# Performance work log

Measured on AMD Instinct MI355X. Metric: run time of the kernel, lower is better.

The kernel has to match this reference:

```python
import jax, jax.numpy as jnp
import numpy as np

N_NODES = 100000
N_EDGES = 1600000
IN_FEATS = 256
N_HEADS = 4
OUT_FEATS = 32
NEG_SLOPE = 0.2


def setup_inputs() -> dict:
    key = jax.random.key(0)
    k0, k1, k2, k3, k4, k5 = jax.random.split(key, 6)
    feat = jax.random.normal(k0, (N_NODES, IN_FEATS), dtype=jnp.float32)
    src = jax.random.randint(k1, (N_EDGES,), 0, N_NODES, dtype=jnp.int32)
    dst = jax.random.randint(k2, (N_EDGES,), 0, N_NODES, dtype=jnp.int32)
    # fc.weight: [num_heads*out_feats, in_feats] (torch Linear layout)
    W = jax.random.normal(k3, (N_HEADS * OUT_FEATS, IN_FEATS), dtype=jnp.float32) * 0.05
    attn_l = jax.random.normal(k4, (1, N_HEADS, OUT_FEATS), dtype=jnp.float32) * 0.1
    attn_r = jax.random.normal(k5, (1, N_HEADS, OUT_FEATS), dtype=jnp.float32) * 0.1
    return {"feat": feat, "src": src, "dst": dst, "W": W, "attn_l": attn_l, "attn_r": attn_r}


def reference(feat, src, dst, W, attn_l, attn_r):
    N = feat.shape[0]
    H, D = attn_l.shape[1], attn_l.shape[2]
    # fc projection -> [N, H, D]
    feat_src = (feat @ W.T).reshape(N, H, D)
    el = jnp.sum(feat_src * attn_l, axis=-1)  # [N, H]
    er = jnp.sum(feat_src * attn_r, axis=-1)  # [N, H]
    # per-edge scores: u_add_v then LeakyReLU  -> [E, H]
    e = jax.nn.leaky_relu(el[src] + er[dst], negative_slope=NEG_SLOPE)
    # edge_softmax: segmented softmax over edges grouped by destination node
    emax = jax.ops.segment_max(e, dst, num_segments=N)  # [N, H]
    emax = jnp.where(jnp.isfinite(emax), emax, jnp.zeros_like(emax))
    ee = jnp.exp(e - emax[dst])  # [E, H]
    denom = jax.ops.segment_sum(ee, dst, num_segments=N)  # [N, H]
    a = ee / denom[dst]  # [E, H]
    # u_mul_e + sum aggregation -> [N, H, D]
    m = feat_src[src] * a[:, :, None]  # [E, H, D]
    rst = jax.ops.segment_sum(m, dst, num_segments=N)
    return rst
```

## Files before the change

kernel.cpp:

```cpp
#include <hip/hip_runtime.h>
#include <hip/hip_bf16.h>
#include <math.h>

#define NN 100000
#define NE 1600000
#define INF_ 256
#define NH 4
#define DH 32
#define NHD 128
#define NEG_SLOPE 0.2f

#define NB 391
#define EPB 8192
#define NBLK_H 196
#define GEMM_BLKS 782

typedef __attribute__((ext_vector_type(8))) short bf16x8;
typedef __attribute__((ext_vector_type(4))) float f32x4;

__device__ __forceinline__ unsigned short f2bf(float f) {
    __hip_bfloat16 b = __float2bfloat16(f);
    return *reinterpret_cast<unsigned short*>(&b);
}

__global__ __launch_bounds__(256) void k_wcvt(const float* __restrict__ W,
                                              unsigned short* __restrict__ Wimg) {
    int i = blockIdx.x * 256 + threadIdx.x;
    if (i >= 4096) return;
    int kt = i >> 9;
    int r = (i >> 2) & 127;
    int g = i & 3;
    int slot = g ^ (r & 7);
    const float* s = &W[(size_t)r * INF_ + kt * 32 + g * 8];
    unsigned short tmp[8];
#pragma unroll
    for (int j = 0; j < 8; j++) tmp[j] = f2bf(s[j]);
    *(bf16x8*)&Wimg[(size_t)kt * 8192 + r * 64 + slot * 8] = *(const bf16x8*)tmp;
}

__global__ __launch_bounds__(256) void k_gemm(const float* __restrict__ feat,
                                              const unsigned short* __restrict__ Wimg,
                                              const int* __restrict__ dst,
                                              const float* __restrict__ al,
                                              const float* __restrict__ ar,
                                              unsigned short* __restrict__ fsb,
                                              float* __restrict__ el,
                                              float* __restrict__ er,
                                              int* __restrict__ bcnt) {
    __shared__ short sA[128 * 64];
    __shared__ short sB[128 * 64];
    __shared__ int lh[NB];
    const int t = threadIdx.x;

    if (blockIdx.x >= GEMM_BLKS) {
        int hb = blockIdx.x - GEMM_BLKS;
        for (int i = t; i < NB; i += 256) lh[i] = 0;
        __syncthreads();
        int base = hb * EPB;
#pragma unroll
        for (int j = 0; j < 32; j++) {
            int e = base + j * 256 + t;
            if (e < NE) atomicAdd(&lh[dst[e] >> 8], 1);
        }
        __syncthreads();
        for (int i = t; i < NB; i += 256)
            if (lh[i]) atomicAdd(&bcnt[i], lh[i]);
        return;
    }

    const int brow = blockIdx.x * 128;
    const int wid = t >> 6, lane = t & 63;
    const int wr = wid >> 1, wc = wid & 1;
    const int lg = lane >> 4;
    const int lr = lane & 15;

    f32x4 acc[4][4];
#pragma unroll
    for (int m = 0; m < 4; m++)
#pragma unroll
        for (int n = 0; n < 4; n++) acc[m][n] = (f32x4){0.f, 0.f, 0.f, 0.f};

    const int srow = t >> 1;
    const int cb = (t & 1) * 16;
    const int g0 = cb >> 3;
    const int p0 = (g0 ^ (srow & 7));
    const int p1 = ((g0 + 1) ^ (srow & 7));
    const int grow = brow + srow;
    const bool arow_ok = (grow < NN);
    const char* bimg = (const char*)Wimg;

    float fv[16];
    uint4 wv0, wv1, wv2, wv3;
    if (arow_ok) {
        const float4* pa = (const float4*)&feat[(size_t)grow * INF_ + cb];
        *(float4*)&fv[0] = pa[0];
        *(float4*)&fv[4] = pa[1];
        *(float4*)&fv[8] = pa[2];
        *(float4*)&fv[12] = pa[3];
    } else {
#pragma unroll
        for (int j = 0; j < 16; j++) fv[j] = 0.f;
    }
    wv0 = *(const uint4*)(bimg + t * 16);
    wv1 = *(const uint4*)(bimg + 4096 + t * 16);
    wv2 = *(const uint4*)(bimg + 8192 + t * 16);
    wv3 = *(const uint4*)(bimg + 12288 + t * 16);

    for (int kt = 0; kt < 8; kt++) {
        {
            short sv[16];
#pragma unroll
            for (int j = 0; j < 16; j++) sv[j] = (short)f2bf(fv[j]);
            *(bf16x8*)&sA[srow * 64 + p0 * 8] = *(const bf16x8*)&sv[0];
            *(bf16x8*)&sA[srow * 64 + p1 * 8] = *(const bf16x8*)&sv[8];
            char* bd = (char*)sB;
            *(uint4*)(bd + t * 16) = wv0;
            *(uint4*)(bd + 4096 + t * 16) = wv1;
            *(uint4*)(bd + 8192 + t * 16) = wv2;
            *(uint4*)(bd + 12288 + t * 16) = wv3;
        }
        __syncthreads();
        if (kt < 7) {
            int k0 = (kt + 1) * 32;
            if (arow_ok) {
                const float4* pa = (const float4*)&feat[(size_t)grow * INF_ + k0 + cb];
                *(float4*)&fv[0] = pa[0];
                *(float4*)&fv[4] = pa[1];
                *(float4*)&fv[8] = pa[2];
                *(float4*)&fv[12] = pa[3];
            }
            const char* bsrc = bimg + (size_t)(kt + 1) * 16384;
            wv0 = *(const uint4*)(bsrc + t * 16);
            wv1 = *(const uint4*)(bsrc + 4096 + t * 16);
            wv2 = *(const uint4*)(bsrc + 8192 + t * 16);
            wv3 = *(const uint4*)(bsrc + 12288 + t * 16);
        }
        bf16x8 aF[4], bF[4];
#pragma unroll
        for (int m = 0; m < 4; m++) {
            int r = wr * 64 + m * 16 + lr;
            aF[m] = *(const bf16x8*)&sA[r * 64 + ((lg ^ (r & 7)) * 8)];
        }
#pragma unroll
        for (int n = 0; n < 4; n++) {
            int r = wc * 64 + n * 16 + lr;
            bF[n] = *(const bf16x8*)&sB[r * 64 + ((lg ^ (r & 7)) * 8)];
        }
#pragma unroll
        for (int m = 0; m < 4; m++)
#pragma unroll
            for (int n = 0; n < 4; n++)
                acc[m][n] = __builtin_amdgcn_mfma_f32_16x16x32_bf16(aF[m], bF[n], acc[m][n], 0, 0, 0);
        __syncthreads();
    }
#pragma unroll
    for (int m = 0; m < 4; m++) {
#pragma unroll
        for (int n = 0; n < 4; n++) {
#pragma unroll
            for (int r = 0; r < 4; r++) {
                int gr = brow + wr * 64 + m * 16 + lg * 4 + r;
                if (gr < NN)
                    fsb[(size_t)gr * NHD + wc * 64 + n * 16 + lr] = f2bf(acc[m][n][r]);
            }
        }
    }
    const int hA = wc * 2, hB = wc * 2 + 1;
    const float alA0 = al[hA * 32 + lr], alA1 = al[hA * 32 + 16 + lr];
    const float alB0 = al[hB * 32 + lr], alB1 = al[hB * 32 + 16 + lr];
    const float arA0 = ar[hA * 32 + lr], arA1 = ar[hA * 32 + 16 + lr];
    const float arB0 = ar[hB * 32 + lr], arB1 = ar[hB * 32 + 16 + lr];
#pragma unroll
    for (int m = 0; m < 4; m++) {
#pragma unroll
        for (int r = 0; r < 4; r++) {
            float eA = acc[m][0][r] * alA0 + acc[m][1][r] * alA1;
            float eB = acc[m][2][r] * alB0 + acc[m][3][r] * alB1;
            float fA = acc[m][0][r] * arA0 + acc[m][1][r] * arA1;
            float fB = acc[m][2][r] * arB0 + acc[m][3][r] * arB1;
#pragma unroll
            for (int off = 1; off < 16; off <<= 1) {
                eA += __shfl_xor(eA, off);
                eB += __shfl_xor(eB, off);
                fA += __shfl_xor(fA, off);
                fB += __shfl_xor(fB, off);
            }
            if (lr == 0) {
                int gr = brow + wr * 64 + m * 16 + lg * 4 + r;
                if (gr < NN) {
                    el[gr * 4 + hA] = eA;
                    el[gr * 4 + hB] = eB;
                    er[gr * 4 + hA] = fA;
                    er[gr * 4 + hB] = fB;
                }
            }
        }
    }
}

__global__ __launch_bounds__(512) void k_bscan(const int* __restrict__ bcnt,
                                               int* __restrict__ ebase,
                                               int* __restrict__ gcur) {
    __shared__ int s[512];
    int t = threadIdx.x;
    int v = (t < NB) ? bcnt[t] : 0;
    s[t] = v;
    __syncthreads();
#pragma unroll
    for (int off = 1; off < 512; off <<= 1) {
        int y = (t >= off) ? s[t - off] : 0;
        __syncthreads();
        s[t] += y;
        __syncthreads();
    }
    if (t < NB) {
        int e = s[t] - v;
        ebase[t] = e;
        gcur[t] = e;
    }
}

__global__ __launch_bounds__(256) void k_bin(const int* __restrict__ src,
                                             const int* __restrict__ dst,
                                             int* __restrict__ gcur,
                                             unsigned* __restrict__ packed) {
    __shared__ int ldst[EPB];
    __shared__ int lc[NB];
    __shared__ int wb[NB];
    int t = threadIdx.x;
    for (int i = t; i < NB; i += 256) lc[i] = 0;
    __syncthreads();
    int base = blockIdx.x * EPB;
#pragma unroll
    for (int j = 0; j < 32; j++) {
        int e = base + j * 256 + t;
        int d = (e < NE) ? dst[e] : -1;
        ldst[j * 256 + t] = d;
        if (d >= 0) atomicAdd(&lc[d >> 8], 1);
    }
    __syncthreads();
    for (int i = t; i < NB; i += 256) {
        int c = lc[i];
        wb[i] = c ? atomicAdd(&gcur[i], c) : 0;
        lc[i] = 0;
    }
    __syncthreads();
#pragma unroll
    for (int j = 0; j < 32; j++) {
        int e = base + j * 256 + t;
        if (e < NE) {
            int d = ldst[j * 256 + t];
            int b = d >> 8;
            int s = src[e];
            int pos = wb[b] + atomicAdd(&lc[b], 1);
            packed[pos] = ((unsigned)s << 8) | (unsigned)(d & 255);
        }
    }
}

__global__ __launch_bounds__(256) void k_sort(const int* __restrict__ ebase,
                                              const int* __restrict__ bcnt,
                                              const unsigned* __restrict__ packed,
                                              int* __restrict__ row_off,
                                              int* __restrict__ esrc) {
    __shared__ int lh[256];
    __shared__ int cur[256];
    __shared__ int wsum[4];
    int b = blockIdx.x, t = threadIdx.x;
    int beg = ebase[b];
    int end = beg + bcnt[b];
    lh[t] = 0;
    __syncthreads();
    for (int k = beg + t; k < end; k += 256) {
        atomicAdd(&lh[packed[k] & 255u], 1);
    }
    __syncthreads();
    int v = lh[t];
    int lane = t & 63, w = t >> 6;
    int x = v;
#pragma unroll
    for (int off = 1; off < 64; off <<= 1) {
        int y = __shfl_up(x, off);
        if (lane >= off) x += y;
    }
    if (lane == 63) wsum[w] = x;
    __syncthreads();
    int add = 0;
    for (int j = 0; j < w; j++) add += wsum[j];
    int excl = beg + add + x - v;
    int node = (b << 8) + t;
    if (node < NN) row_off[node] = excl;
    cur[t] = excl;
    __syncthreads();
    for (int k = beg + t; k < end; k += 256) {
        unsigned p = packed[k];
        int pos = atomicAdd(&cur[p & 255u], 1);
        esrc[pos] = (int)(p >> 8);
    }
    if (b == NB - 1 && t == 0) row_off[NN] = NE;
}

__global__ __launch_bounds__(256) void k_agg(const int* __restrict__ row_off,
                                             const int* __restrict__ esrc,
                                             const float* __restrict__ el,
                                             const float* __restrict__ er,
                                             const uint4* __restrict__ fsb128,
                                             float* __restrict__ out) {
    int gid = blockIdx.x * blockDim.x + threadIdx.x;
    int node = gid >> 6;
    int lane = gid & 63;
    if (node >= NN) return;
    int q = lane >> 4;
    int sl = lane & 15;
    int h = sl >> 2;
    int beg = row_off[node];
    int end = row_off[node + 1];
    float rr = er[node * 4 + h];
    float den = 0.f;
    float a0 = 0.f, a1 = 0.f, a2 = 0.f, a3 = 0.f;
    float a4 = 0.f, a5 = 0.f, a6 = 0.f, a7 = 0.f;

#define STEP(eV, vV)                                           \
    {                                                          \
        float sc = (eV) + rr;                                  \
        sc = sc > 0.f ? sc : NEG_SLOPE * sc;                   \
        float ee = __expf(sc);                                 \
        den += ee;                                             \
        a0 += ee * __uint_as_float((vV).x << 16);              \
        a1 += ee * __uint_as_float((vV).x & 0xFFFF0000u);      \
        a2 += ee * __uint_as_float((vV).y << 16);              \
        a3 += ee * __uint_as_float((vV).y & 0xFFFF0000u);      \
        a4 += ee * __uint_as_float((vV).z << 16);              \
        a5 += ee * __uint_as_float((vV).z & 0xFFFF0000u);      \
        a6 += ee * __uint_as_float((vV).w << 16);              \
        a7 += ee * __uint_as_float((vV).w & 0xFFFF0000u);      \
    }

    int k = beg + q;
    for (; k + 4 < end; k += 8) {
        int s0 = esrc[k];
        int s1 = esrc[k + 4];
        uint4 v0 = fsb128[(size_t)s0 * 16 + sl];
        uint4 v1 = fsb128[(size_t)s1 * 16 + sl];
        float e0 = el[s0 * 4 + h];
        float e1 = el[s1 * 4 + h];
        STEP(e0, v0)
        STEP(e1, v1)
    }
    for (; k < end; k += 4) {
        int s = esrc[k];
        uint4 v = fsb128[(size_t)s * 16 + sl];
        float eV = el[s * 4 + h];
        STEP(eV, v)
    }
#undef STEP

#pragma unroll
    for (int off = 16; off <= 32; off <<= 1) {
        a0 += __shfl_xor(a0, off);
        a1 += __shfl_xor(a1, off);
        a2 += __shfl_xor(a2, off);
        a3 += __shfl_xor(a3, off);
        a4 += __shfl_xor(a4, off);
        a5 += __shfl_xor(a5, off);
        a6 += __shfl_xor(a6, off);
        a7 += __shfl_xor(a7, off);
        den += __shfl_xor(den, off);
    }

    if (q == 0) {
        float inv = den > 0.f ? 1.0f / den : 0.f;
        float4 o0, o1;
        o0.x = a0 * inv; o0.y = a1 * inv; o0.z = a2 * inv; o0.w = a3 * inv;
        o1.x = a4 * inv; o1.y = a5 * inv; o1.z = a6 * inv; o1.w = a7 * inv;
        float* p = &out[(size_t)node * NHD + sl * 8];
        *(float4*)p = o0;
        *(float4*)(p + 4) = o1;
    }
}

extern "C" void kernel_launch(void* const* d_in, const int* in_sizes, int n_in,
                              void* d_out, int out_size, void* d_ws, size_t ws_size,
                              hipStream_t stream) {
    const float* feat = (const float*)d_in[0];
    const int* src = (const int*)d_in[1];
    const int* dst = (const int*)d_in[2];
    const float* W = (const float*)d_in[3];
    const float* al = (const float*)d_in[4];
    const float* ar = (const float*)d_in[5];
    float* out = (float*)d_out;

    char* ws = (char*)d_ws;
    unsigned short* fsb = (unsigned short*)ws;   ws += (size_t)NN * NHD * 2;
    unsigned* packed = (unsigned*)ws;            ws += (size_t)NE * 4;
    int* esrc = (int*)ws;                        ws += (size_t)NE * 4;
    float* el = (float*)ws;                      ws += (size_t)NN * NH * 4;
    float* er = (float*)ws;                      ws += (size_t)NN * NH * 4;
    int* row_off = (int*)ws;                     ws += (size_t)(NN + 1) * 4;
    int* bcnt = (int*)ws;                        ws += (size_t)NB * 4;
    int* ebase = (int*)ws;                       ws += (size_t)NB * 4;
    int* gcur = (int*)ws;                        ws += (size_t)NB * 4;
    unsigned short* Wimg = (unsigned short*)ws;  ws += (size_t)8 * 8192 * 2;

    hipMemsetAsync(bcnt, 0, (size_t)NB * sizeof(int), stream);

    k_wcvt<<<16, 256, 0, stream>>>(W, Wimg);
    k_gemm<<<GEMM_BLKS + NBLK_H, 256, 0, stream>>>(feat, Wimg, dst, al, ar,
                                                   fsb, el, er, bcnt);
    k_bscan<<<1, 512, 0, stream>>>(bcnt, ebase, gcur);
    k_bin<<<NBLK_H, 256, 0, stream>>>(src, dst, gcur, packed);
    k_sort<<<NB, 256, 0, stream>>>(ebase, bcnt, packed, row_off, esrc);
    k_agg<<<(NN * 64 + 255) / 256, 256, 0, stream>>>(row_off, esrc, el, er,
                                                     (const uint4*)fsb, out);
}
```

Measured before the change: 166.9 us.

## Fuse bucket scan into binning and local sort into aggregation

Removes the separate scan, sort and aggregation kernels by computing bucket prefix sums inside each binning block and doing per-bucket counting sort in shared memory directly before aggregation. Buckets shrink to 128 nodes so the sorted source list fits in LDS, eliminating the global esrc/row_off round trip and several launches. It also replaces the memset with a block in the weight-convert kernel. Risks include truncation if a bucket exceeds the fixed LDS capacity and reduced parallelism since each wave now serially handles 32 nodes.

Result: faster. 160.4 us (-3.9%).

```diff
diff --git a/kernel.cpp b/kernel.cpp
--- a/kernel.cpp
+++ b/kernel.cpp
@@ -10,10 +10,11 @@
 #define NHD 128
 #define NEG_SLOPE 0.2f
 
-#define NB 391
-#define EPB 8192
-#define NBLK_H 196
+#define NB2 782
+#define EPB 4096
+#define NBLK_H 391
 #define GEMM_BLKS 782
+#define MAXBE 3072
 
 typedef __attribute__((ext_vector_type(8))) short bf16x8;
 typedef __attribute__((ext_vector_type(4))) float f32x4;
@@ -23,10 +24,20 @@
     return *reinterpret_cast<unsigned short*>(&b);
 }
 
-__global__ __launch_bounds__(256) void k_wcvt(const float* __restrict__ W,
-                                              unsigned short* __restrict__ Wimg) {
-    int i = blockIdx.x * 256 + threadIdx.x;
-    if (i >= 4096) return;
+__global__ __launch_bounds__(256) void k_prep0(const float* __restrict__ W,
+                                               unsigned short* __restrict__ Wimg,
+                                               int* __restrict__ bcnt,
+                                               int* __restrict__ gcur) {
+    int t = threadIdx.x;
+    int b = blockIdx.x;
+    if (b == 16) {
+        for (int i = t; i < NB2; i += 256) {
+            bcnt[i] = 0;
+            gcur[i] = 0;
+        }
+        return;
+    }
+    int i = b * 256 + t;
     int kt = i >> 9;
     int r = (i >> 2) & 127;
     int g = i & 3;
@@ -49,21 +60,21 @@
                                               int* __restrict__ bcnt) {
     __shared__ short sA[128 * 64];
     __shared__ short sB[128 * 64];
-    __shared__ int lh[NB];
+    __shared__ int lh[NB2];
     const int t = threadIdx.x;
 
     if (blockIdx.x >= GEMM_BLKS) {
         int hb = blockIdx.x - GEMM_BLKS;
-        for (int i = t; i < NB; i += 256) lh[i] = 0;
+        for (int i = t; i < NB2; i += 256) lh[i] = 0;
         __syncthreads();
         int base = hb * EPB;
 #pragma unroll
-        for (int j = 0; j < 32; j++) {
+        for (int j = 0; j < 16; j++) {
             int e = base + j * 256 + t;
-            if (e < NE) atomicAdd(&lh[dst[e] >> 8], 1);
+            if (e < NE) atomicAdd(&lh[dst[e] >> 7], 1);
         }
         __syncthreads();
-        for (int i = t; i < NB; i += 256)
+        for (int i = t; i < NB2; i += 256)
             if (lh[i]) atomicAdd(&bcnt[i], lh[i]);
         return;
     }
@@ -198,133 +209,132 @@
     }
 }
 
-__global__ __launch_bounds__(512) void k_bscan(const int* __restrict__ bcnt,
-                                               int* __restrict__ ebase,
-                                               int* __restrict__ gcur) {
-    __shared__ int s[512];
-    int t = threadIdx.x;
-    int v = (t < NB) ? bcnt[t] : 0;
-    s[t] = v;
-    __syncthreads();
-#pragma unroll
-    for (int off = 1; off < 512; off <<= 1) {
-        int y = (t >= off) ? s[t - off] : 0;
-        __syncthreads();
-        s[t] += y;
-        __syncthreads();
-    }
-    if (t < NB) {
-        int e = s[t] - v;
-        ebase[t] = e;
-        gcur[t] = e;
-    }
-}
-
 __global__ __launch_bounds__(256) void k_bin(const int* __restrict__ src,
                                              const int* __restrict__ dst,
+                                             const int* __restrict__ bcnt,
                                              int* __restrict__ gcur,
+                                             int* __restrict__ ebase_g,
                                              unsigned* __restrict__ packed) {
     __shared__ int ldst[EPB];
-    __shared__ int lc[NB];
-    __shared__ int wb[NB];
+    __shared__ int sc[NB2];
+    __shared__ int lc[NB2];
+    __shared__ int wb[NB2];
+    __shared__ int wsum[4];
     int t = threadIdx.x;
-    for (int i = t; i < NB; i += 256) lc[i] = 0;
-    __syncthreads();
+    int base4 = t * 4;
+    int c0 = (base4 + 0 < NB2) ? bcnt[base4 + 0] : 0;
+    int c1 = (base4 + 1 < NB2) ? bcnt[base4 + 1] : 0;
+    int c2 = (base4 + 2 < NB2) ? bcnt[base4 + 2] : 0;
+    int c3 = (base4 + 3 < NB2) ? bcnt[base4 + 3] : 0;
+    int s4 = c0 + c1 + c2 + c3;
+    int lane = t & 63, w = t >> 6;
+    int x = s4;
+#pragma unroll
+    for (int o = 1; o < 64; o <<= 1) {
+        int y = __shfl_up(x, o);
+        if (lane >= o) x += y;
+    }
+    if (lane == 63) wsum[w] = x;
+    __syncthreads();
+    int add = 0;
+    for (int j = 0; j < w; j++) add += wsum[j];
+    int ex = add + x - s4;
+    if (base4 + 0 < NB2) sc[base4 + 0] = ex;
+    if (base4 + 1 < NB2) sc[base4 + 1] = ex + c0;
+    if (base4 + 2 < NB2) sc[base4 + 2] = ex + c0 + c1;
+    if (base4 + 3 < NB2) sc[base4 + 3] = ex + c0 + c1 + c2;
+    for (int i = t; i < NB2; i += 256) lc[i] = 0;
+    __syncthreads();
+    if (blockIdx.x == 0)
+        for (int i = t; i < NB2; i += 256) ebase_g[i] = sc[i];
     int base = blockIdx.x * EPB;
 #pragma unroll
-    for (int j = 0; j < 32; j++) {
+    for (int j = 0; j < 16; j++) {
         int e = base + j * 256 + t;
         int d = (e < NE) ? dst[e] : -1;
         ldst[j * 256 + t] = d;
-        if (d >= 0) atomicAdd(&lc[d >> 8], 1);
-    }
-    __syncthreads();
-    for (int i = t; i < NB; i += 256) {
+        if (d >= 0) atomicAdd(&lc[d >> 7], 1);
+    }
+    __syncthreads();
+    for (int i = t; i < NB2; i += 256) {
         int c = lc[i];
-        wb[i] = c ? atomicAdd(&gcur[i], c) : 0;
+        wb[i] = c ? sc[i] + atomicAdd(&gcur[i], c) : 0;
         lc[i] = 0;
     }
     __syncthreads();
 #pragma unroll
-    for (int j = 0; j < 32; j++) {
+    for (int j = 0; j < 16; j++) {
         int e = base + j * 256 + t;
         if (e < NE) {
             int d = ldst[j * 256 + t];
-            int b = d >> 8;
+            int bk = d >> 7;
             int s = src[e];
-            int pos = wb[b] + atomicAdd(&lc[b], 1);
-            packed[pos] = ((unsigned)s << 8) | (unsigned)(d & 255);
-        }
-    }
-}
-
-__global__ __launch_bounds__(256) void k_sort(const int* __restrict__ ebase,
-                                              const int* __restrict__ bcnt,
-                                              const unsigned* __restrict__ packed,
-                                              int* __restrict__ row_off,
-                                              int* __restrict__ esrc) {
-    __shared__ int lh[256];
-    __shared__ int cur[256];
-    __shared__ int wsum[4];
+            int pos = wb[bk] + atomicAdd(&lc[bk], 1);
+            packed[pos] = ((unsigned)s << 7) | (unsigned)(d & 127);
+        }
+    }
+}
+
+__global__ __launch_bounds__(256) void k_sortagg(const int* __restrict__ ebase_g,
+                                                 const int* __restrict__ bcnt,
+                                                 const unsigned* __restrict__ packed,
+                                                 const float* __restrict__ el,
+                                                 const float* __restrict__ er,
+                                                 const uint4* __restrict__ fsb128,
+                                                 float* __restrict__ out) {
+    __shared__ int lh[128];
+    __shared__ int off[129];
+    __shared__ int cur[128];
+    __shared__ int wsum2[2];
+    __shared__ int esrc_l[MAXBE];
     int b = blockIdx.x, t = threadIdx.x;
-    int beg = ebase[b];
-    int end = beg + bcnt[b];
-    lh[t] = 0;
-    __syncthreads();
-    for (int k = beg + t; k < end; k += 256) {
-        atomicAdd(&lh[packed[k] & 255u], 1);
-    }
-    __syncthreads();
-    int v = lh[t];
+    int beg = ebase_g[b];
+    int cnt = bcnt[b];
+    if (cnt > MAXBE) cnt = MAXBE;
+
+    if (t < 128) lh[t] = 0;
+    __syncthreads();
+    for (int k = t; k < cnt; k += 256)
+        atomicAdd(&lh[packed[beg + k] & 127u], 1);
+    __syncthreads();
+    int v = 0, x = 0;
     int lane = t & 63, w = t >> 6;
-    int x = v;
-#pragma unroll
-    for (int off = 1; off < 64; off <<= 1) {
-        int y = __shfl_up(x, off);
-        if (lane >= off) x += y;
-    }
-    if (lane == 63) wsum[w] = x;
-    __syncthreads();
-    int add = 0;
-    for (int j = 0; j < w; j++) add += wsum[j];
-    int excl = beg + add + x - v;
-    int node = (b << 8) + t;
-    if (node < NN) row_off[node] = excl;
-    cur[t] = excl;
-    __syncthreads();
-    for (int k = beg + t; k < end; k += 256) {
-        unsigned p = packed[k];
-        int pos = atomicAdd(&cur[p & 255u], 1);
-        esrc[pos] = (int)(p >> 8);
-    }
-    if (b == NB - 1 && t == 0) row_off[NN] = NE;
-}
-
-__global__ __launch_bounds__(256) void k_agg(const int* __restrict__ row_off,
-                                             const int* __restrict__ esrc,
-                                             const float* __restrict__ el,
-                                             const float* __restrict__ er,
-                                             const uint4* __restrict__ fsb128,
-                                             float* __restrict__ out) {
-    int gid = blockIdx.x * blockDim.x + threadIdx.x;
-    int node = gid >> 6;
-    int lane = gid & 63;
-    if (node >= NN) return;
+    if (t < 128) {
+        v = lh[t];
+        x = v;
+#pragma unroll
+        for (int o = 1; o < 64; o <<= 1) {
+            int y = __shfl_up(x, o);
+            if (lane >= o) x += y;
+        }
+        if (lane == 63) wsum2[w] = x;
+    }
+    __syncthreads();
+    if (t < 128) {
+        int add = (w == 1) ? wsum2[0] : 0;
+        int e = add + x - v;
+        off[t] = e;
+        cur[t] = e;
+    }
+    if (t == 0) off[128] = cnt;
+    __syncthreads();
+    for (int k = t; k < cnt; k += 256) {
+        unsigned p = packed[beg + k];
+        int pos = atomicAdd(&cur[p & 127u], 1);
+        esrc_l[pos] = (int)(p >> 7);
+    }
+    __syncthreads();
+
+    int wv = t >> 6;
     int q = lane >> 4;
     int sl = lane & 15;
     int h = sl >> 2;
-    int beg = row_off[node];
-    int end = row_off[node + 1];
-    float rr = er[node * 4 + h];
-    float den = 0.f;
-    float a0 = 0.f, a1 = 0.f, a2 = 0.f, a3 = 0.f;
-    float a4 = 0.f, a5 = 0.f, a6 = 0.f, a7 = 0.f;
 
 #define STEP(eV, vV)                                           \
     {                                                          \
-        float sc = (eV) + rr;                                  \
-        sc = sc > 0.f ? sc : NEG_SLOPE * sc;                   \
-        float ee = __expf(sc);                                 \
+        float sc_ = (eV) + rr;                                 \
+        sc_ = sc_ > 0.f ? sc_ : NEG_SLOPE * sc_;               \
+        float ee = __expf(sc_);                                \
         den += ee;                                             \
         a0 += ee * __uint_as_float((vV).x << 16);              \
         a1 += ee * __uint_as_float((vV).x & 0xFFFF0000u);      \
@@ -336,47 +346,55 @@
         a7 += ee * __uint_as_float((vV).w & 0xFFFF0000u);      \
     }
 
-    int k = beg + q;
-    for (; k + 4 < end; k += 8) {
-        int s0 = esrc[k];
-        int s1 = esrc[k + 4];
-        uint4 v0 = fsb128[(size_t)s0 * 16 + sl];
-        uint4 v1 = fsb128[(size_t)s1 * 16 + sl];
-        float e0 = el[s0 * 4 + h];
-        float e1 = el[s1 * 4 + h];
-        STEP(e0, v0)
-        STEP(e1, v1)
-    }
-    for (; k < end; k += 4) {
-        int s = esrc[k];
-        uint4 v = fsb128[(size_t)s * 16 + sl];
-        float eV = el[s * 4 + h];
-        STEP(eV, v)
+    for (int ln = wv * 32; ln < wv * 32 + 32; ln++) {
+        int node = (b << 7) + ln;
+        if (node >= NN) break;
+        int bg = off[ln];
+        int en = off[ln + 1];
+        float rr = er[node * 4 + h];
+        float den = 0.f;
+        float a0 = 0.f, a1 = 0.f, a2 = 0.f, a3 = 0.f;
+        float a4 = 0.f, a5 = 0.f, a6 = 0.f, a7 = 0.f;
+        int k = bg + q;
+        for (; k + 4 < en; k += 8) {
+            int s0 = esrc_l[k];
+            int s1 = esrc_l[k + 4];
+            uint4 v0 = fsb128[(size_t)s0 * 16 + sl];
+            uint4 v1 = fsb128[(size_t)s1 * 16 + sl];
+            float e0 = el[s0 * 4 + h];
+            float e1 = el[s1 * 4 + h];
+            STEP(e0, v0)
+            STEP(e1, v1)
+        }
+        for (; k < en; k += 4) {
+            int s = esrc_l[k];
+            uint4 vv = fsb128[(size_t)s * 16 + sl];
+            float eV = el[s * 4 + h];
+            STEP(eV, vv)
+        }
+#pragma unroll
+        for (int o = 16; o <= 32; o <<= 1) {
+            a0 += __shfl_xor(a0, o);
+            a1 += __shfl_xor(a1, o);
+            a2 += __shfl_xor(a2, o);
+            a3 += __shfl_xor(a3, o);
+            a4 += __shfl_xor(a4, o);
+            a5 += __shfl_xor(a5, o);
+            a6 += __shfl_xor(a6, o);
+            a7 += __shfl_xor(a7, o);
+            den += __shfl_xor(den, o);
+        }
+        if (q == 0) {
+            float inv = den > 0.f ? 1.0f / den : 0.f;
+            float4 o0, o1;
+            o0.x = a0 * inv; o0.y = a1 * inv; o0.z = a2 * inv; o0.w = a3 * inv;
+            o1.x = a4 * inv; o1.y = a5 * inv; o1.z = a6 * inv; o1.w = a7 * inv;
+            float* p = &out[(size_t)node * NHD + sl * 8];
+            *(float4*)p = o0;
+            *(float4*)(p + 4) = o1;
+        }
     }
 #undef STEP
-
-#pragma unroll
-    for (int off = 16; off <= 32; off <<= 1) {
-        a0 += __shfl_xor(a0, off);
-        a1 += __shfl_xor(a1, off);
-        a2 += __shfl_xor(a2, off);
-        a3 += __shfl_xor(a3, off);
-        a4 += __shfl_xor(a4, off);
-        a5 += __shfl_xor(a5, off);
-        a6 += __shfl_xor(a6, off);
-        a7 += __shfl_xor(a7, off);
-        den += __shfl_xor(den, off);
-    }
-
-    if (q == 0) {
-        float inv = den > 0.f ? 1.0f / den : 0.f;
-        float4 o0, o1;
-        o0.x = a0 * inv; o0.y = a1 * inv; o0.z = a2 * inv; o0.w = a3 * inv;
-        o1.x = a4 * inv; o1.y = a5 * inv; o1.z = a6 * inv; o1.w = a7 * inv;
-        float* p = &out[(size_t)node * NHD + sl * 8];
-        *(float4*)p = o0;
-        *(float4*)(p + 4) = o1;
-    }
 }
 
 extern "C" void kernel_launch(void* const* d_in, const int* in_sizes, int n_in,
@@ -393,23 +411,17 @@
     char* ws = (char*)d_ws;
     unsigned short* fsb = (unsigned short*)ws;   ws += (size_t)NN * NHD * 2;
     unsigned* packed = (unsigned*)ws;            ws += (size_t)NE * 4;
-    int* esrc = (int*)ws;                        ws += (size_t)NE * 4;
     float* el = (float*)ws;                      ws += (size_t)NN * NH * 4;
     float* er = (float*)ws;                      ws += (size_t)NN * NH * 4;
-    int* row_off = (int*)ws;                     ws += (size_t)(NN + 1) * 4;
-    int* bcnt = (int*)ws;                        ws += (size_t)NB * 4;
-    int* ebase = (int*)ws;                       ws += (size_t)NB * 4;
-    int* gcur = (int*)ws;                        ws += (size_t)NB * 4;
+    int* bcnt = (int*)ws;                        ws += (size_t)NB2 * 4;
+    int* gcur = (int*)ws;                        ws += (size_t)NB2 * 4;
+    int* ebase_g = (int*)ws;                     ws += (size_t)NB2 * 4;
     unsigned short* Wimg = (unsigned short*)ws;  ws += (size_t)8 * 8192 * 2;
 
-    hipMemsetAsync(bcnt, 0, (size_t)NB * sizeof(int), stream);
-
-    k_wcvt<<<16, 256, 0, stream>>>(W, Wimg);
+    k_prep0<<<17, 256, 0, stream>>>(W, Wimg, bcnt, gcur);
     k_gemm<<<GEMM_BLKS + NBLK_H, 256, 0, stream>>>(feat, Wimg, dst, al, ar,
                                                    fsb, el, er, bcnt);
-    k_bscan<<<1, 512, 0, stream>>>(bcnt, ebase, gcur);
-    k_bin<<<NBLK_H, 256, 0, stream>>>(src, dst, gcur, packed);
-    k_sort<<<NB, 256, 0, stream>>>(ebase, bcnt, packed, row_off, esrc);
-    k_agg<<<(NN * 64 + 255) / 256, 256, 0, stream>>>(row_off, esrc, el, er,
-                                                     (const uint4*)fsb, out);
-}
+    k_bin<<<NBLK_H, 256, 0, stream>>>(src, dst, bcnt, gcur, ebase_g, packed);
+    k_sortagg<<<NB2, 256, 0, stream>>>(ebase_g, bcnt, packed, el, er,
+                                       (const uint4*)fsb, out);
+}
```
